# Kernel optimization log

Measured on AMD Instinct MI355X. Metric: run time of the kernel, lower is better.

The kernel has to match this reference:

```python
import jax, jax.numpy as jnp
import numpy as np

# Production-scale dims (see shape_source)
B, C, H, W = 4, 128, 64, 64
RADIUS = 0.2
TEMP = 0.1
PAD_VALUE = 0.0
P = int(H * RADIUS) * 2 + 1  # local window size kH = kW = 25


def setup_inputs() -> dict:
    key = jax.random.key(0)
    k1, k2 = jax.random.split(key)
    query = jax.random.normal(k1, (B, C, H, W), dtype=jnp.float32)
    keys = jax.random.normal(k2, (B, C, H, W), dtype=jnp.float32)
    return {"query": query, "keys": keys}


def _make_idx_map(h_dim, w_dim, p):
    # Equivalent of F.unfold(arange(H*W).view(H,W), kernel=(P,P), pad=P//2).clamp(min=0)
    # idx[h, w, p1, p2] = linear index of (h+p1-P//2, w+p2-P//2), 0 if out of bounds
    off = np.arange(p) - p // 2
    hh = np.arange(h_dim)[:, None, None, None] + off[None, None, :, None]  # (H,1,P,1)
    ww = np.arange(w_dim)[None, :, None, None] + off[None, None, None, :]  # (1,W,1,P)
    valid = (hh >= 0) & (hh < h_dim) & (ww >= 0) & (ww < w_dim)
    idx = np.where(valid, hh * w_dim + ww, 0)  # (H,W,P,P)
    return jnp.asarray(idx.reshape(h_dim * w_dim, p * p), dtype=jnp.int32)

_IDX_MAP = _make_idx_map(H, W, P)  # (H*W, P*P) int32 constant


def _local_correlation(query, keys, p):
    # spatial_correlation_sample(kernel=1, patch=P, stride=1, pad=0, dilation=1):
    # att[b,p1,p2,h,w] = sum_c query[b,c,h,w] * keys_zero_padded[b,c,h+p1-P//2,w+p2-P//2]
    pad = p // 2
    keys_pad = jnp.pad(keys, ((0, 0), (0, 0), (pad, pad), (pad, pad)))

    def corr_one(i):
        p1, p2 = i // p, i % p
        k = jax.lax.dynamic_slice(keys_pad, (0, 0, p1, p2), keys.shape)
        return jnp.einsum('bchw,bchw->bhw', query, k)

    att = jax.lax.map(corr_one, jnp.arange(p * p))  # (P*P, B, H, W); sequential keeps memory low
    return jnp.transpose(att, (1, 2, 3, 0))  # b h w (p1 p2)


def reference(query, keys):
    n_pix = H * W
    att = _local_correlation(query, keys, P) / TEMP  # (B,H,W,P*P)
    # knn(): pad_value==0, topk==0 -> mask exact zeros (out-of-window zero-padded corrs) to -10
    A = jnp.where(att == PAD_VALUE, jnp.float32(-10.0), att)
    A = jnp.exp(A.reshape(B, n_pix, P * P))  # b (h w) n
    # scatter_add into dense (B, H*W, H*W) affinity map
    q_idx = jnp.arange(n_pix)[:, None]  # (HW,1)
    out = jnp.zeros((B, n_pix, n_pix), dtype=A.dtype)
    out = out.at[:, q_idx, _IDX_MAP].add(A)
    # rearr 'b (h w) n -> b n h w'
    return out.reshape(B, H, W, n_pix).transpose(0, 3, 1, 2)
```

## Files before the change

### kernel.cpp

```cpp
#include <hip/hip_runtime.h>
#include <math.h>
#include <float.h>


#define BDIM 256
constexpr int Bn = 4, Cc = 128, Hh = 64, Ww = 64, HW = 4096;
constexpr int P = 25, Rr = 12, T = 8;

__device__ __forceinline__ int cntf(int x) {
    int c = P;
    if (x < Rr) c -= (Rr - x);
    if (x > (Hh - 1 - Rr)) c -= (x - (Hh - 1 - Rr));
    return c;
}

__global__ __launch_bounds__(BDIM) void localwalk_kernel(
    const float* __restrict__ query, const float* __restrict__ keys,
    float* __restrict__ out)
{
    const int jt  = blockIdx.x;
    const int jh  = blockIdx.y;
    const int b   = blockIdx.z;
    const int jw0 = jt * T;
    const int t   = threadIdx.x;

    __shared__ float Klds[Cc][T];

    const float E10 = expf(-10.0f);

    float* orow = out + ((size_t)(b * HW + jh * Ww + jw0)) * HW;
    if (jh == 0 && jw0 == 0) {
        for (int i = t; i < HW; i += BDIM) {
            int h = i >> 6, w = i & 63;
            float ninv = (float)(P * P - cntf(h) * cntf(w));
            orow[i] = ninv * E10;
        }
        float4 z4 = make_float4(0.f, 0.f, 0.f, 0.f);
        float4* o4 = (float4*)(orow + HW);
        for (int i = t; i < 7 * (HW / 4); i += BDIM) o4[i] = z4;
    } else {
        float4 z4 = make_float4(0.f, 0.f, 0.f, 0.f);
        float4* o4 = (float4*)orow;
        for (int i = t; i < 8 * (HW / 4); i += BDIM) o4[i] = z4;
    }

    const float* kb = keys + (size_t)b * Cc * HW + jh * Ww + jw0;
    for (int i = t; i < Cc * T; i += BDIM) {
        int c = i >> 3, jj = i & 7;
        Klds[c][jj] = kb[(size_t)c * HW + jj];
    }
    __syncthreads();

    const int wloc = t & 31;
    const int hs   = t >> 5;
    const int w    = jw0 - Rr + wloc;
    const int wa   = min(max(w, 0), Ww - 1);
    const bool wvalid = (w >= 0) && (w < Ww);

    int ha[4]; bool hv[4];
    #pragma unroll
    for (int r = 0; r < 4; ++r) {
        int hloc = hs + 8 * r;
        int h = jh - Rr + hloc;
        hv[r] = (hloc < P) && (h >= 0) && (h < Hh);
        ha[r] = min(max(h, 0), Hh - 1);
    }

    float acc[4][T];
    #pragma unroll
    for (int r = 0; r < 4; ++r)
        #pragma unroll
        for (int jj = 0; jj < T; ++jj) acc[r][jj] = 0.f;

    const float* qb = query + (size_t)b * Cc * HW;
    int qoff[4];
    #pragma unroll
    for (int r = 0; r < 4; ++r) qoff[r] = ha[r] * Ww + wa;

    #pragma unroll 2
    for (int c = 0; c < Cc; ++c) {
        const float* qc = qb + (size_t)c * HW;
        float qv[4];
        #pragma unroll
        for (int r = 0; r < 4; ++r) qv[r] = qc[qoff[r]];
        float4 k0 = *(const float4*)&Klds[c][0];
        float4 k1 = *(const float4*)&Klds[c][4];
        float kk[T] = {k0.x, k0.y, k0.z, k0.w, k1.x, k1.y, k1.z, k1.w};
        #pragma unroll
        for (int jj = 0; jj < T; ++jj)
            #pragma unroll
            for (int r = 0; r < 4; ++r)
                acc[r][jj] = fmaf(qv[r], kk[jj], acc[r][jj]);
    }

    #pragma unroll
    for (int r = 0; r < 4; ++r) {
        if (!hv[r] || !wvalid) continue;
        const int h = ha[r];
        #pragma unroll
        for (int jj = 0; jj < T; ++jj) {
            int d = wloc - jj;
            if (d < 0 || d > 2 * Rr) continue;
            float att = acc[r][jj] / 0.1f;
            if (att == 0.0f) att = -10.0f;
            att = fminf(att, 88.0f);
            float e = expf(att);
            int j = jh * Ww + jw0 + jj;
            if (j == 0) {
                float ninv = (float)(P * P - cntf(h) * cntf(w));
                e += ninv * E10;
            }
            out[((size_t)(b * HW + j)) * HW + h * Ww + w] = e;
        }
    }
}

extern "C" void kernel_launch(void* const* d_in, const int* in_sizes, int n_in,
                              void* d_out, int out_size, void* d_ws, size_t ws_size,
                              hipStream_t stream) {
    const float* query = (const float*)d_in[0];
    const float* keys  = (const float*)d_in[1];
    float* out = (float*)d_out;
    dim3 grid(Ww / T, Hh, Bn);
    localwalk_kernel<<<grid, dim3(BDIM), 0, stream>>>(query, keys, out);
}
```

Before: 404.4 us.

## Interleave output zero-fill stores with the channel reduction loop

The up-front zero-fill of each block's eight output rows is moved into the channel loop, issuing one float4 store every fourth channel, so the large write stream overlaps the query loads and FMAs instead of preceding them. A barrier is added before the final scatter of exp values so the fill is complete before those entries are overwritten. The channel loop unroll goes from 2 to 4, and the writeback loop is reordered to iterate rows first. This adds register pressure and a block-wide sync in exchange for better overlap of the store-bound fill with compute.

```diff
diff --git a/kernel.cpp b/kernel.cpp
--- a/kernel.cpp
+++ b/kernel.cpp
@@ -27,22 +27,7 @@
     __shared__ float Klds[Cc][T];
 
     const float E10 = expf(-10.0f);
-
-    float* orow = out + ((size_t)(b * HW + jh * Ww + jw0)) * HW;
-    if (jh == 0 && jw0 == 0) {
-        for (int i = t; i < HW; i += BDIM) {
-            int h = i >> 6, w = i & 63;
-            float ninv = (float)(P * P - cntf(h) * cntf(w));
-            orow[i] = ninv * E10;
-        }
-        float4 z4 = make_float4(0.f, 0.f, 0.f, 0.f);
-        float4* o4 = (float4*)(orow + HW);
-        for (int i = t; i < 7 * (HW / 4); i += BDIM) o4[i] = z4;
-    } else {
-        float4 z4 = make_float4(0.f, 0.f, 0.f, 0.f);
-        float4* o4 = (float4*)orow;
-        for (int i = t; i < 8 * (HW / 4); i += BDIM) o4[i] = z4;
-    }
+    const bool special = (jh == 0) && (jt == 0);
 
     const float* kb = keys + (size_t)b * Cc * HW + jh * Ww + jw0;
     for (int i = t; i < Cc * T; i += BDIM) {
@@ -77,7 +62,9 @@
     #pragma unroll
     for (int r = 0; r < 4; ++r) qoff[r] = ha[r] * Ww + wa;
 
-    #pragma unroll 2
+    float4* orow4 = (float4*)(out + ((size_t)(b * HW + jh * Ww + jw0)) * HW);
+
+    #pragma unroll 4
     for (int c = 0; c < Cc; ++c) {
         const float* qc = qb + (size_t)c * HW;
         float qv[4];
@@ -85,6 +72,22 @@
         for (int r = 0; r < 4; ++r) qv[r] = qc[qoff[r]];
         float4 k0 = *(const float4*)&Klds[c][0];
         float4 k1 = *(const float4*)&Klds[c][4];
+
+        if ((c & 3) == 0) {
+            const int fi = t + (c >> 2) * BDIM;
+            float4 v = make_float4(0.f, 0.f, 0.f, 0.f);
+            if (special && fi < 1024) {
+                int e0 = fi * 4;
+                int h = e0 >> 6, w0 = e0 & 63;
+                int ch = cntf(h);
+                v.x = (float)(P * P - ch * cntf(w0 + 0)) * E10;
+                v.y = (float)(P * P - ch * cntf(w0 + 1)) * E10;
+                v.z = (float)(P * P - ch * cntf(w0 + 2)) * E10;
+                v.w = (float)(P * P - ch * cntf(w0 + 3)) * E10;
+            }
+            orow4[fi] = v;
+        }
+
         float kk[T] = {k0.x, k0.y, k0.z, k0.w, k1.x, k1.y, k1.z, k1.w};
         #pragma unroll
         for (int jj = 0; jj < T; ++jj)
@@ -93,24 +96,27 @@
                 acc[r][jj] = fmaf(qv[r], kk[jj], acc[r][jj]);
     }
 
+    __syncthreads();
+
     #pragma unroll
-    for (int r = 0; r < 4; ++r) {
-        if (!hv[r] || !wvalid) continue;
-        const int h = ha[r];
+    for (int jj = 0; jj < T; ++jj) {
+        const int d = wloc - jj;
+        const bool dv = (d >= 0) && (d <= 2 * Rr) && wvalid;
+        float* obase = out + ((size_t)(b * HW + jh * Ww + jw0 + jj)) * HW;
+        const bool isj0 = special && (jj == 0);
         #pragma unroll
-        for (int jj = 0; jj < T; ++jj) {
-            int d = wloc - jj;
-            if (d < 0 || d > 2 * Rr) continue;
+        for (int r = 0; r < 4; ++r) {
+            if (!dv || !hv[r]) continue;
+            const int h = ha[r];
             float att = acc[r][jj] / 0.1f;
             if (att == 0.0f) att = -10.0f;
             att = fminf(att, 88.0f);
             float e = expf(att);
-            int j = jh * Ww + jw0 + jj;
-            if (j == 0) {
+            if (isj0) {
                 float ninv = (float)(P * P - cntf(h) * cntf(w));
                 e += ninv * E10;
             }
-            out[((size_t)(b * HW + j)) * HW + h * Ww + w] = e;
+            obase[h * Ww + w] = e;
         }
     }
 }
```

After: 447.3 us. 10.6% more time.
